# Optimization experiments

Hardware: AMD Instinct MI355X
Metric: run time of the kernel (lower is better)

The kernel has to match this reference:

```python
import jax, jax.numpy as jnp
import numpy as np

RHO = 1.0


def _cayley():
    # Geometric-product structure constants for Cl(2,0), basis (1, e1, e2, e12).
    C = np.zeros((4, 4, 4), dtype=np.float32)
    entries = [
        (0, 0, 0, 1), (0, 1, 1, 1), (0, 2, 2, 1), (0, 3, 3, 1),
        (1, 0, 1, 1), (1, 1, 0, 1), (1, 2, 3, 1), (1, 3, 2, 1),
        (2, 0, 2, 1), (2, 1, 3, -1), (2, 2, 0, 1), (2, 3, 1, -1),
        (3, 0, 3, 1), (3, 1, 2, -1), (3, 2, 1, 1), (3, 3, 0, -1),
    ]
    for x, y, z, s in entries:
        C[x, y, z] = s
    return jnp.asarray(C)

CAYLEY = _cayley()

B, I, O, G, X = 64, 64, 64, 4096, 4
GRID_MIN, GRID_MAX = -2.0, 2.0


def setup_inputs() -> dict:
    key = jax.random.key(0)
    k1, k2, k3 = jax.random.split(key, 3)
    x = jax.random.normal(k1, (B, I, X), dtype=jnp.float32)
    # random_grid: quasirandom points in [grid_min, grid_max]^X (Sobol in torch; uniform here)
    grid = jax.random.uniform(k2, (G, X), dtype=jnp.float32) * (GRID_MAX - GRID_MIN) + GRID_MIN
    weights = jax.random.normal(k3, (I, O, G, X), dtype=jnp.float32)
    silu_weight = jnp.ones((I, O, X), dtype=jnp.float32)
    silu_bias = jnp.zeros((I, O, X), dtype=jnp.float32)
    return {"x": x, "grid": grid, "weights": weights,
            "silu_weight": silu_weight, "silu_bias": silu_bias}


def reference(x, grid, weights, silu_weight, silu_bias):
    # x: (B, I, X); grid: (G, X); weights: (I, O, G, X)
    diff = x[:, :, None, :] - grid[None, None, :, :]          # (B, I, G, X)
    # algebra.norm(v)**2 with Euclidean metric = sum over multivector components
    rbf = jnp.exp(-jnp.sum(diff * diff, axis=-1) / RHO)       # (B, I, G)
    result = jnp.einsum('big,iogx->biox', rbf, weights)       # (B, I, O, X)
    # componentwise SiLU branch: geometric product via cayley tensor
    sx = jax.nn.silu(x)                                       # (B, I, X)
    silu_val = jnp.einsum('iox,biy,xyz->bioz', silu_weight, sx, CAYLEY)
    silu_val = silu_val + silu_bias                           # broadcast (B, I, O, X)
    out = jnp.sum(result + silu_val, axis=1)                  # 'biox->box'
    return out                                                # NoNorm: identity norm
```

## Files before the change

kernel.cpp:

```cpp
#include <hip/hip_runtime.h>
#include <hip/hip_bf16.h>

#define BB 64
#define II 64
#define OO 64
#define GG 4096
#define KP 32
#define NCH 8
#define GC (GG / NCH)
#define NPH (GC / KP)
#define NSL (II * NCH)

typedef short bf16x8 __attribute__((ext_vector_type(8)));
typedef short bf16x4 __attribute__((ext_vector_type(4)));
typedef float f32x4  __attribute__((ext_vector_type(4)));
typedef unsigned short u16x4 __attribute__((ext_vector_type(4)));

static __device__ __forceinline__ short f2bf(float f) {
    __hip_bfloat16 h = __float2bfloat16(f);
    return __builtin_bit_cast(short, h);
}
static __device__ __forceinline__ unsigned short f2bfu(float f) {
    __hip_bfloat16 h = __float2bfloat16(f);
    return __builtin_bit_cast(unsigned short, h);
}
static __device__ __forceinline__ float bfu2f(unsigned short u) {
    unsigned int v = (unsigned int)u << 16;
    return __builtin_bit_cast(float, v);
}

__global__ __launch_bounds__(512, 4)
void kan_main(const float* __restrict__ xg, const float* __restrict__ grd,
              const float* __restrict__ wts, unsigned short* __restrict__ dst,
              float* __restrict__ fdst, int atomic_mode)
{
    __shared__ __align__(16) float          Wst[2][OO * KP * 4];
    __shared__ __align__(16) unsigned short As [2][BB * KP];
    __shared__ __align__(16) float4         Gs [GC];

    const int i  = blockIdx.x;
    const int ch = blockIdx.y;
    const int g0 = ch * GC;
    const int s  = (i + ch) & (NPH - 1);

    const int t    = threadIdx.x;
    const int lane = t & 63;
    const int wv   = t >> 6;

    const int brow = t >> 3;
    const int gq   = t & 7;
    const float4 xv = reinterpret_cast<const float4*>(xg)[brow * II + i];

    {
        const float4* gsrc = reinterpret_cast<const float4*>(grd) + g0 + t;
        char* ldst = (char*)(&Gs[0]) + wv * 1024;
        __builtin_amdgcn_global_load_lds(gsrc, ldst, 16, 0, 0);
    }

    const float4* w4 = reinterpret_cast<const float4*>(wts)
                       + (size_t)i * OO * GG;
    const int srow_half = lane >> 5;
    const int su        = lane & 31;

    #pragma unroll
    for (int q = 0; q < 4; ++q) {
        const int rr = 2 * (q * 8 + wv) + srow_half;
        const int gg = g0 + s * KP + (su ^ (rr & 7));
        __builtin_amdgcn_global_load_lds(w4 + (size_t)rr * GG + gg,
            (char*)(&Wst[0][0]) + (q * 8 + wv) * 1024, 16, 0, 0);
    }

    asm volatile("s_waitcnt vmcnt(4)\n\ts_barrier" ::: "memory");

    f32x4 acc[4][2];
    #pragma unroll
    for (int mt = 0; mt < 4; ++mt)
        #pragma unroll
        for (int nt = 0; nt < 2; ++nt) acc[mt][nt] = {0.f, 0.f, 0.f, 0.f};

    const int lg    = lane >> 4;
    const int r16   = lane & 15;
    const int bo_lo = r16 >> 2;
    const int bx    = r16 & 3;

    for (int p = 0; p < NPH; ++p) {
        const int b  = p & 1;
        const int cp = (p + s) & (NPH - 1);
        const int np = (p + 1 + s) & (NPH - 1);

        if (p + 1 < NPH) {
            #pragma unroll
            for (int q = 0; q < 4; ++q) {
                const int rr = 2 * (q * 8 + wv) + srow_half;
                const int gg = g0 + np * KP + (su ^ (rr & 7));
                __builtin_amdgcn_global_load_lds(w4 + (size_t)rr * GG + gg,
                    (char*)(&Wst[b ^ 1][0]) + (q * 8 + wv) * 1024, 16, 0, 0);
            }
        }

        {
            bf16x4 av;
            #pragma unroll
            for (int e = 0; e < 4; ++e) {
                const float4 gv = Gs[cp * KP + gq * 4 + e];
                const float d0 = xv.x - gv.x, d1 = xv.y - gv.y,
                            d2 = xv.z - gv.z, d3 = xv.w - gv.w;
                av[e] = f2bf(__expf(-(d0*d0 + d1*d1 + d2*d2 + d3*d3)));
            }
            *reinterpret_cast<bf16x4*>(
                &As[b][brow * KP + ((gq * 4) ^ ((brow & 3) << 3))]) = av;
        }

        if (p + 1 < NPH)
            asm volatile("s_waitcnt vmcnt(4) lgkmcnt(0)\n\ts_barrier" ::: "memory");
        else
            asm volatile("s_waitcnt vmcnt(0) lgkmcnt(0)\n\ts_barrier" ::: "memory");

        bf16x8 af[4];
        #pragma unroll
        for (int mt = 0; mt < 4; ++mt) {
            const int r = mt * 16 + r16;
            af[mt] = *reinterpret_cast<const bf16x8*>(
                &As[b][r * KP + ((lg * 8) ^ ((r & 3) << 3))]);
        }
        bf16x8 bb[2];
        #pragma unroll
        for (int nt = 0; nt < 2; ++nt) {
            const int o  = wv * 8 + nt * 4 + bo_lo;
            const int sg = o & 7;
            const float* bp = &Wst[b][o * 128 + bx];
            #pragma unroll
            for (int e = 0; e < 8; ++e)
                bb[nt][e] = f2bf(bp[(lg * 8 + (e ^ sg)) * 4]);
        }
        #pragma unroll
        for (int mt = 0; mt < 4; ++mt)
            #pragma unroll
            for (int nt = 0; nt < 2; ++nt)
                acc[mt][nt] = __builtin_amdgcn_mfma_f32_16x16x32_bf16(
                    af[mt], bb[nt], acc[mt][nt], 0, 0, 0);

        asm volatile("s_waitcnt lgkmcnt(0)\n\ts_barrier" ::: "memory");
    }

    if (!atomic_mode) {
        unsigned short* pd = dst + (size_t)(ch * 64 + i) * (BB * OO * 4);
        #pragma unroll
        for (int mt = 0; mt < 4; ++mt)
            #pragma unroll
            for (int nt = 0; nt < 2; ++nt) {
                const int n  = wv * 32 + nt * 16 + (lane & 15);
                const int mb = mt * 16 + ((lane >> 4) << 2);
                #pragma unroll
                for (int r = 0; r < 4; ++r)
                    pd[(mb + r) * 256 + n] = f2bfu(acc[mt][nt][r]);
            }
    } else {
        #pragma unroll
        for (int mt = 0; mt < 4; ++mt)
            #pragma unroll
            for (int nt = 0; nt < 2; ++nt) {
                const int n  = wv * 32 + nt * 16 + (lane & 15);
                const int mb = mt * 16 + ((lane >> 4) << 2);
                #pragma unroll
                for (int r = 0; r < 4; ++r)
                    atomicAdd(&fdst[(mb + r) * 256 + n], acc[mt][nt][r]);
            }
    }
}

__global__ __launch_bounds__(256)
void kan_tail(const unsigned short* __restrict__ part,
              const float* __restrict__ xg,
              const float* __restrict__ sw,
              const float* __restrict__ sb,
              float* __restrict__ out)
{
    __shared__ float4 sums[16][16];

    const int t     = threadIdx.x;
    const int bid   = blockIdx.x;
    const int pairL = t & 15;
    const int rgrp  = t >> 4;
    const int pairG = bid * 16 + pairL;

    const u16x4* p4 = reinterpret_cast<const u16x4*>(part);
    float4 s = make_float4(0.f, 0.f, 0.f, 0.f);
    #pragma unroll 8
    for (int k = 0; k < 32; ++k) {
        const u16x4 v = p4[(size_t)(rgrp * 32 + k) * 4096 + pairG];
        s.x += bfu2f(v[0]); s.y += bfu2f(v[1]);
        s.z += bfu2f(v[2]); s.w += bfu2f(v[3]);
    }
    sums[pairL][rgrp] = s;
    __syncthreads();

    if (t < 16) {
        const int pg = bid * 16 + t;
        const int b = pg >> 6, o = pg & 63;

        float o0 = 0.f, o1 = 0.f, o2 = 0.f, o3 = 0.f;
        #pragma unroll
        for (int r = 0; r < 16; ++r) {
            const float4 v = sums[t][r];
            o0 += v.x; o1 += v.y; o2 += v.z; o3 += v.w;
        }

        const float4* xg4 = reinterpret_cast<const float4*>(xg);
        const float4* sw4 = reinterpret_cast<const float4*>(sw);
        const float4* sb4 = reinterpret_cast<const float4*>(sb);
        #pragma unroll 4
        for (int i = 0; i < II; ++i) {
            const float4 xvv = xg4[b * II + i];
            const float4 swv = sw4[i * OO + o];
            const float4 sbv = sb4[i * OO + o];
            const float s0 = xvv.x / (1.f + __expf(-xvv.x));
            const float s1 = xvv.y / (1.f + __expf(-xvv.y));
            const float s2 = xvv.z / (1.f + __expf(-xvv.z));
            const float s3 = xvv.w / (1.f + __expf(-xvv.w));
            o0 += swv.x * s0 + swv.y * s1 + swv.z * s2 - swv.w * s3 + sbv.x;
            o1 += swv.x * s1 + swv.y * s0 - swv.z * s3 + swv.w * s2 + sbv.y;
            o2 += swv.x * s2 + swv.y * s3 + swv.z * s0 - swv.w * s1 + sbv.z;
            o3 += swv.x * s3 + swv.y * s2 - swv.z * s1 + swv.w * s0 + sbv.w;
        }
        reinterpret_cast<float4*>(out)[pg] = make_float4(o0, o1, o2, o3);
    }
}

__global__ void kan_out(const float* __restrict__ xg,
                        const float* __restrict__ sw,
                        const float* __restrict__ sb,
                        float* __restrict__ out)
{
    const int t = blockIdx.x * 256 + threadIdx.x;
    const int b = t >> 6, o = t & 63;

    const float4 v = reinterpret_cast<const float4*>(out)[t];
    float o0 = v.x, o1 = v.y, o2 = v.z, o3 = v.w;

    const float4* xg4 = reinterpret_cast<const float4*>(xg);
    const float4* sw4 = reinterpret_cast<const float4*>(sw);
    const float4* sb4 = reinterpret_cast<const float4*>(sb);
    #pragma unroll 4
    for (int i = 0; i < II; ++i) {
        const float4 xvv = xg4[b * II + i];
        const float4 swv = sw4[i * OO + o];
        const float4 sbv = sb4[i * OO + o];
        const float s0 = xvv.x / (1.f + __expf(-xvv.x));
        const float s1 = xvv.y / (1.f + __expf(-xvv.y));
        const float s2 = xvv.z / (1.f + __expf(-xvv.z));
        const float s3 = xvv.w / (1.f + __expf(-xvv.w));
        o0 += swv.x * s0 + swv.y * s1 + swv.z * s2 - swv.w * s3 + sbv.x;
        o1 += swv.x * s1 + swv.y * s0 - swv.z * s3 + swv.w * s2 + sbv.y;
        o2 += swv.x * s2 + swv.y * s3 + swv.z * s0 - swv.w * s1 + sbv.z;
        o3 += swv.x * s3 + swv.y * s2 - swv.z * s1 + swv.w * s0 + sbv.w;
    }
    reinterpret_cast<float4*>(out)[t] = make_float4(o0, o1, o2, o3);
}

extern "C" void kernel_launch(void* const* d_in, const int* in_sizes, int n_in,
                              void* d_out, int out_size, void* d_ws, size_t ws_size,
                              hipStream_t stream)
{
    const float* x   = (const float*)d_in[0];
    const float* grd = (const float*)d_in[1];
    const float* w   = (const float*)d_in[2];
    const float* sw  = (const float*)d_in[3];
    const float* sb  = (const float*)d_in[4];
    float* out = (float*)d_out;

    const size_t need = (size_t)NSL * 16384 * 2;

    if (ws_size >= need) {
        unsigned short* ws = (unsigned short*)d_ws;
        kan_main<<<dim3(64, NCH), 512, 0, stream>>>(x, grd, w, ws, nullptr, 0);
        kan_tail<<<256, 256, 0, stream>>>(ws, x, sw, sb, out);
    } else {
        hipMemsetAsync(d_out, 0, (size_t)out_size * sizeof(float), stream);
        kan_main<<<dim3(64, NCH), 512, 0, stream>>>(x, grd, w, nullptr, out, 1);
        kan_out<<<16, 256, 0, stream>>>(x, sw, sb, out);
    }
}
```

Baseline: 72.46 us.

## Split main GEMM over output halves and grid quarters with K=64 phases

Changes the main kernel decomposition from (input, 8 grid chunks) to (input, 2 output halves, 4 grid quarters). Each block now processes 64-wide K phases on 32 output rows, and the RBF activations for the next phase are computed in registers while the current MFMA runs. Grid points are streamed per phase into a small LDS buffer instead of loading a whole chunk up front. The partial layout and the tail reduction are adjusted to match. The trade is that each block now recomputes the RBF activations for its own output half, so the exp work doubles in exchange for less LDS use and more overlap.

```diff
diff --git a/kernel.cpp b/kernel.cpp
--- a/kernel.cpp
+++ b/kernel.cpp
@@ -5,14 +5,11 @@
 #define II 64
 #define OO 64
 #define GG 4096
-#define KP 32
-#define NCH 8
-#define GC (GG / NCH)
-#define NPH (GC / KP)
-#define NSL (II * NCH)
+#define KP 64
+#define NPH 16
+#define NSL 512
 
 typedef short bf16x8 __attribute__((ext_vector_type(8)));
-typedef short bf16x4 __attribute__((ext_vector_type(4)));
 typedef float f32x4  __attribute__((ext_vector_type(4)));
 typedef unsigned short u16x4 __attribute__((ext_vector_type(4)));
 
@@ -34,54 +31,64 @@
               const float* __restrict__ wts, unsigned short* __restrict__ dst,
               float* __restrict__ fdst, int atomic_mode)
 {
-    __shared__ __align__(16) float          Wst[2][OO * KP * 4];
-    __shared__ __align__(16) unsigned short As [2][BB * KP];
-    __shared__ __align__(16) float4         Gs [GC];
-
-    const int i  = blockIdx.x;
-    const int ch = blockIdx.y;
-    const int g0 = ch * GC;
-    const int s  = (i + ch) & (NPH - 1);
+    __shared__ __align__(16) float          Wst[2][32 * 256];
+    __shared__ __align__(16) unsigned short As [BB * KP];
+    __shared__ __align__(16) float4         Gs [KP];
+
+    const int i   = blockIdx.x;
+    const int oc  = blockIdx.y;
+    const int gch = blockIdx.z;
+    const int s   = (i + 4 * gch + 8 * oc) & (NPH - 1);
 
     const int t    = threadIdx.x;
     const int lane = t & 63;
     const int wv   = t >> 6;
 
     const int brow = t >> 3;
-    const int gq   = t & 7;
+    const int oct  = t & 7;
     const float4 xv = reinterpret_cast<const float4*>(xg)[brow * II + i];
 
-    {
-        const float4* gsrc = reinterpret_cast<const float4*>(grd) + g0 + t;
-        char* ldst = (char*)(&Gs[0]) + wv * 1024;
-        __builtin_amdgcn_global_load_lds(gsrc, ldst, 16, 0, 0);
-    }
-
     const float4* w4 = reinterpret_cast<const float4*>(wts)
-                       + (size_t)i * OO * GG;
-    const int srow_half = lane >> 5;
-    const int su        = lane & 31;
-
+        + ((size_t)i * OO + oc * 32) * GG + (size_t)gch * 1024;
+    const float4* g4 = reinterpret_cast<const float4*>(grd) + gch * 1024;
+    const int qs_hi = (lane >> 3) & 1;
+
+    __builtin_amdgcn_global_load_lds(g4 + s * KP + lane, (char*)(&Gs[0]),
+                                     16, 0, 0);
     #pragma unroll
     for (int q = 0; q < 4; ++q) {
-        const int rr = 2 * (q * 8 + wv) + srow_half;
-        const int gg = g0 + s * KP + (su ^ (rr & 7));
-        __builtin_amdgcn_global_load_lds(w4 + (size_t)rr * GG + gg,
-            (char*)(&Wst[0][0]) + (q * 8 + wv) * 1024, 16, 0, 0);
-    }
-
-    asm volatile("s_waitcnt vmcnt(4)\n\ts_barrier" ::: "memory");
-
-    f32x4 acc[4][2];
+        const int rr = q * 8 + wv;
+        const int qs = ((rr & 3) << 1) | qs_hi;
+        __builtin_amdgcn_global_load_lds(
+            w4 + (size_t)rr * GG + s * KP + (lane ^ qs),
+            (char*)(&Wst[0][0]) + rr * 1024, 16, 0, 0);
+    }
+    asm volatile("s_waitcnt vmcnt(4)" ::: "memory");
+
+    {
+        bf16x8 pa;
+        #pragma unroll
+        for (int e = 0; e < 8; ++e) {
+            const float4 g = Gs[oct * 8 + e];
+            const float d0 = xv.x - g.x, d1 = xv.y - g.y,
+                        d2 = xv.z - g.z, d3 = xv.w - g.w;
+            pa[e] = f2bf(__expf(-(d0*d0 + d1*d1 + d2*d2 + d3*d3)));
+        }
+        *reinterpret_cast<bf16x8*>(
+            &As[brow * KP + ((oct * 8) ^ ((brow & 7) << 3))]) = pa;
+    }
+    asm volatile("s_waitcnt lgkmcnt(0)\n\ts_barrier" ::: "memory");
+    __builtin_amdgcn_global_load_lds(g4 + ((s + 1) & (NPH - 1)) * KP + lane,
+                                     (char*)(&Gs[0]), 16, 0, 0);
+
+    f32x4 acc[4];
     #pragma unroll
-    for (int mt = 0; mt < 4; ++mt)
-        #pragma unroll
-        for (int nt = 0; nt < 2; ++nt) acc[mt][nt] = {0.f, 0.f, 0.f, 0.f};
-
-    const int lg    = lane >> 4;
-    const int r16   = lane & 15;
-    const int bo_lo = r16 >> 2;
-    const int bx    = r16 & 3;
+    for (int mt = 0; mt < 4; ++mt) acc[mt] = {0.f, 0.f, 0.f, 0.f};
+
+    const int lg   = lane >> 4;
+    const int r16  = lane & 15;
+    const int orow = wv * 4 + (r16 >> 2);
+    const int bx   = r16 & 3;
 
     for (int p = 0; p < NPH; ++p) {
         const int b  = p & 1;
@@ -91,81 +98,81 @@
         if (p + 1 < NPH) {
             #pragma unroll
             for (int q = 0; q < 4; ++q) {
-                const int rr = 2 * (q * 8 + wv) + srow_half;
-                const int gg = g0 + np * KP + (su ^ (rr & 7));
-                __builtin_amdgcn_global_load_lds(w4 + (size_t)rr * GG + gg,
-                    (char*)(&Wst[b ^ 1][0]) + (q * 8 + wv) * 1024, 16, 0, 0);
-            }
-        }
-
-        {
-            bf16x4 av;
-            #pragma unroll
-            for (int e = 0; e < 4; ++e) {
-                const float4 gv = Gs[cp * KP + gq * 4 + e];
-                const float d0 = xv.x - gv.x, d1 = xv.y - gv.y,
-                            d2 = xv.z - gv.z, d3 = xv.w - gv.w;
-                av[e] = f2bf(__expf(-(d0*d0 + d1*d1 + d2*d2 + d3*d3)));
-            }
-            *reinterpret_cast<bf16x4*>(
-                &As[b][brow * KP + ((gq * 4) ^ ((brow & 3) << 3))]) = av;
+                const int rr = q * 8 + wv;
+                const int qs = ((rr & 3) << 1) | qs_hi;
+                __builtin_amdgcn_global_load_lds(
+                    w4 + (size_t)rr * GG + np * KP + (lane ^ qs),
+                    (char*)(&Wst[b ^ 1][0]) + rr * 1024, 16, 0, 0);
+            }
         }
 
         if (p + 1 < NPH)
-            asm volatile("s_waitcnt vmcnt(4) lgkmcnt(0)\n\ts_barrier" ::: "memory");
+            asm volatile("s_waitcnt vmcnt(4)" ::: "memory");
         else
-            asm volatile("s_waitcnt vmcnt(0) lgkmcnt(0)\n\ts_barrier" ::: "memory");
-
-        bf16x8 af[4];
-        #pragma unroll
-        for (int mt = 0; mt < 4; ++mt) {
-            const int r = mt * 16 + r16;
-            af[mt] = *reinterpret_cast<const bf16x8*>(
-                &As[b][r * KP + ((lg * 8) ^ ((r & 3) << 3))]);
-        }
-        bf16x8 bb[2];
-        #pragma unroll
-        for (int nt = 0; nt < 2; ++nt) {
-            const int o  = wv * 8 + nt * 4 + bo_lo;
-            const int sg = o & 7;
-            const float* bp = &Wst[b][o * 128 + bx];
-            #pragma unroll
-            for (int e = 0; e < 8; ++e)
-                bb[nt][e] = f2bf(bp[(lg * 8 + (e ^ sg)) * 4]);
-        }
+            asm volatile("s_waitcnt vmcnt(0)" ::: "memory");
+
+        bf16x8 pa;
+        if (p + 1 < NPH) {
+            #pragma unroll
+            for (int e = 0; e < 8; ++e) {
+                const float4 g = Gs[oct * 8 + e];
+                const float d0 = xv.x - g.x, d1 = xv.y - g.y,
+                            d2 = xv.z - g.z, d3 = xv.w - g.w;
+                pa[e] = f2bf(__expf(-(d0*d0 + d1*d1 + d2*d2 + d3*d3)));
+            }
+        }
+
+        asm volatile("s_waitcnt lgkmcnt(0)\n\ts_barrier" ::: "memory");
+
+        #pragma unroll
+        for (int kk = 0; kk < 2; ++kk) {
+            bf16x8 bb;
+            #pragma unroll
+            for (int e = 0; e < 8; ++e) {
+                const int g  = kk * 32 + lg * 8 + e;
+                const int qp = ((orow & 3) << 1) | (lg & 1);
+                bb[e] = f2bf(Wst[b][orow * 256 + ((g ^ qp) << 2) + bx]);
+            }
+            #pragma unroll
+            for (int mt = 0; mt < 4; ++mt) {
+                const int rA = mt * 16 + r16;
+                const bf16x8 af = *reinterpret_cast<const bf16x8*>(
+                    &As[rA * KP + ((kk * 32 + lg * 8) ^ ((rA & 7) << 3))]);
+                acc[mt] = __builtin_amdgcn_mfma_f32_16x16x32_bf16(
+                    af, bb, acc[mt], 0, 0, 0);
+            }
+        }
+
+        asm volatile("s_waitcnt lgkmcnt(0)\n\ts_barrier" ::: "memory");
+
+        if (p + 1 < NPH) {
+            *reinterpret_cast<bf16x8*>(
+                &As[brow * KP + ((oct * 8) ^ ((brow & 7) << 3))]) = pa;
+        }
+        if (p + 2 < NPH) {
+            __builtin_amdgcn_global_load_lds(
+                g4 + ((p + 2 + s) & (NPH - 1)) * KP + lane,
+                (char*)(&Gs[0]), 16, 0, 0);
+        }
+    }
+
+    const int nloc = wv * 16 + r16;
+    const int mb   = ((lane >> 4) << 2);
+    if (!atomic_mode) {
+        unsigned short* pd = dst
+            + (size_t)((i * 2 + oc) * 4 + gch) * (BB * 128);
         #pragma unroll
         for (int mt = 0; mt < 4; ++mt)
             #pragma unroll
-            for (int nt = 0; nt < 2; ++nt)
-                acc[mt][nt] = __builtin_amdgcn_mfma_f32_16x16x32_bf16(
-                    af[mt], bb[nt], acc[mt][nt], 0, 0, 0);
-
-        asm volatile("s_waitcnt lgkmcnt(0)\n\ts_barrier" ::: "memory");
-    }
-
-    if (!atomic_mode) {
-        unsigned short* pd = dst + (size_t)(ch * 64 + i) * (BB * OO * 4);
+            for (int r = 0; r < 4; ++r)
+                pd[(mt * 16 + mb + r) * 128 + nloc] = f2bfu(acc[mt][r]);
+    } else {
         #pragma unroll
         for (int mt = 0; mt < 4; ++mt)
             #pragma unroll
-            for (int nt = 0; nt < 2; ++nt) {
-                const int n  = wv * 32 + nt * 16 + (lane & 15);
-                const int mb = mt * 16 + ((lane >> 4) << 2);
-                #pragma unroll
-                for (int r = 0; r < 4; ++r)
-                    pd[(mb + r) * 256 + n] = f2bfu(acc[mt][nt][r]);
-            }
-    } else {
-        #pragma unroll
-        for (int mt = 0; mt < 4; ++mt)
-            #pragma unroll
-            for (int nt = 0; nt < 2; ++nt) {
-                const int n  = wv * 32 + nt * 16 + (lane & 15);
-                const int mb = mt * 16 + ((lane >> 4) << 2);
-                #pragma unroll
-                for (int r = 0; r < 4; ++r)
-                    atomicAdd(&fdst[(mb + r) * 256 + n], acc[mt][nt][r]);
-            }
+            for (int r = 0; r < 4; ++r)
+                atomicAdd(&fdst[(mt * 16 + mb + r) * 256 + oc * 128 + nloc],
+                          acc[mt][r]);
     }
 }
 
@@ -183,21 +190,26 @@
     const int pairL = t & 15;
     const int rgrp  = t >> 4;
     const int pairG = bid * 16 + pairL;
-
-    const u16x4* p4 = reinterpret_cast<const u16x4*>(part);
-    float4 s = make_float4(0.f, 0.f, 0.f, 0.f);
-    #pragma unroll 8
-    for (int k = 0; k < 32; ++k) {
-        const u16x4 v = p4[(size_t)(rgrp * 32 + k) * 4096 + pairG];
-        s.x += bfu2f(v[0]); s.y += bfu2f(v[1]);
-        s.z += bfu2f(v[2]); s.w += bfu2f(v[3]);
-    }
-    sums[pairL][rgrp] = s;
+    const int b     = pairG >> 6, o = pairG & 63;
+    const int oc    = o >> 5;
+
+    float4 s4 = make_float4(0.f, 0.f, 0.f, 0.f);
+    #pragma unroll 4
+    for (int m = 0; m < 16; ++m) {
+        const int idx = rgrp * 16 + m;
+        const int ii  = idx >> 2, gg = idx & 3;
+        const size_t sl = (size_t)((ii * 2 + oc) * 4 + gg);
+        const u16x4 v = *reinterpret_cast<const u16x4*>(
+            part + sl * (BB * 128) + b * 128 + (o & 31) * 4);
+        s4.x += bfu2f(v[0]); s4.y += bfu2f(v[1]);
+        s4.z += bfu2f(v[2]); s4.w += bfu2f(v[3]);
+    }
+    sums[pairL][rgrp] = s4;
     __syncthreads();
 
     if (t < 16) {
         const int pg = bid * 16 + t;
-        const int b = pg >> 6, o = pg & 63;
+        const int bb = pg >> 6, oo = pg & 63;
 
         float o0 = 0.f, o1 = 0.f, o2 = 0.f, o3 = 0.f;
         #pragma unroll
@@ -211,9 +223,9 @@
         const float4* sb4 = reinterpret_cast<const float4*>(sb);
         #pragma unroll 4
         for (int i = 0; i < II; ++i) {
-            const float4 xvv = xg4[b * II + i];
-            const float4 swv = sw4[i * OO + o];
-            const float4 sbv = sb4[i * OO + o];
+            const float4 xvv = xg4[bb * II + i];
+            const float4 swv = sw4[i * OO + oo];
+            const float4 sbv = sb4[i * OO + oo];
             const float s0 = xvv.x / (1.f + __expf(-xvv.x));
             const float s1 = xvv.y / (1.f + __expf(-xvv.y));
             const float s2 = xvv.z / (1.f + __expf(-xvv.z));
@@ -269,15 +281,15 @@
     const float* sb  = (const float*)d_in[4];
     float* out = (float*)d_out;
 
-    const size_t need = (size_t)NSL * 16384 * 2;
+    const size_t need = (size_t)NSL * (BB * 128) * 2;
 
     if (ws_size >= need) {
         unsigned short* ws = (unsigned short*)d_ws;
-        kan_main<<<dim3(64, NCH), 512, 0, stream>>>(x, grd, w, ws, nullptr, 0);
+        kan_main<<<dim3(64, 2, 4), 512, 0, stream>>>(x, grd, w, ws, nullptr, 0);
         kan_tail<<<256, 256, 0, stream>>>(ws, x, sw, sb, out);
     } else {
         hipMemsetAsync(d_out, 0, (size_t)out_size * sizeof(float), stream);
-        kan_main<<<dim3(64, NCH), 512, 0, stream>>>(x, grd, w, nullptr, out, 1);
+        kan_main<<<dim3(64, 2, 4), 512, 0, stream>>>(x, grd, w, nullptr, out, 1);
         kan_out<<<16, 256, 0, stream>>>(x, sw, sb, out);
     }
 }
```

New measurement: 70.59 us. -2.6%, faster.
